# Kernel tuning notes

Measured on AMD Instinct MI355X. Metric: run time of the kernel, lower is better.

The kernel has to match this reference:

```python
import jax, jax.numpy as jnp
import numpy as np
import math

D_MODEL, D_HEAD = 1024, 64
N_HEADS = D_MODEL // D_HEAD  # 16
EPS = 1e-6

def rms_norm(x, scale, eps=EPS):
    ms = jnp.mean(x * x, axis=-1, keepdims=True)
    return x * scale * jax.lax.rsqrt(ms + eps)

def apply_rotary_emb(x, theta):
    # theta: (..., d) rotates first 2*d dims of x
    d = theta.shape[-1]
    x1, x2, x3 = x[..., :d], x[..., d:2 * d], x[..., 2 * d:]
    cos, sin = jnp.cos(theta), jnp.sin(theta)
    return jnp.concatenate([x1 * cos - x2 * sin, x2 * cos + x1 * sin, x3], axis=-1)

def make_freqs():
    d4 = D_HEAD // 4  # 16
    log_min, log_max = math.log(math.pi), math.log(10.0 * math.pi)
    f = np.exp(np.linspace(log_min, log_max, N_HEADS * d4 + 1, dtype=np.float64)[:-1])
    return jnp.asarray(f.reshape(d4, N_HEADS).T, dtype=jnp.float32)  # (n_heads, d_head//4)

def setup_inputs() -> dict:
    key = jax.random.key(0)
    ks = jax.random.split(key, 8)
    n, l = 4, 1024
    x = jax.random.normal(ks[0], (n, l, D_MODEL), jnp.float32)
    pos = jax.random.uniform(ks[1], (n, l, 2), jnp.float32)
    attn_mask = jnp.ones((1, 1, l, l), dtype=bool)
    cond = jax.random.normal(ks[2], (n, 1, D_MODEL), jnp.float32)
    norm_w = jax.random.normal(ks[3], (D_MODEL, D_MODEL), jnp.float32) * 0.02
    qkv_w = jax.random.normal(ks[4], (3 * D_MODEL, D_MODEL), jnp.float32) * (D_MODEL ** -0.5)
    qk_scale = jnp.ones((N_HEADS, 1, 1), jnp.float32)
    out_w = jax.random.normal(ks[5], (D_MODEL, D_MODEL), jnp.float32) * 0.02
    freqs = make_freqs()
    return {"x": x, "pos": pos, "attn_mask": attn_mask, "cond": cond,
            "norm_w": norm_w, "qkv_w": qkv_w, "qk_scale": qk_scale,
            "freqs": freqs, "out_w": out_w}

def reference(x, pos, attn_mask, cond, norm_w, qkv_w, qk_scale, freqs, out_w):
    n, l, d = x.shape
    # AdaRMSNorm
    h = rms_norm(x, jnp.einsum('nlc,dc->nld', cond, norm_w) + 1.0)
    # QKV projection -> (n, h, l, e)
    qkv = jnp.einsum('nld,ed->nle', h, qkv_w)
    q, k, v = jnp.split(qkv, 3, axis=-1)
    split_heads = lambda t: t.reshape(n, l, N_HEADS, D_HEAD).transpose(0, 2, 1, 3)
    q, k, v = split_heads(q), split_heads(k), split_heads(v)
    # per-head RMSNorm (scale shape (h,1,1))
    q = rms_norm(q, qk_scale)
    k = rms_norm(k, qk_scale)
    # axial RoPE: theta (n, h, l, d_head//2)
    theta = jnp.concatenate([
        pos[:, None, :, 0:1] * freqs[None, :, None, :],
        pos[:, None, :, 1:2] * freqs[None, :, None, :],
    ], axis=-1)
    q = apply_rotary_emb(q, theta)
    k = apply_rotary_emb(k, theta)
    # SDPA
    scores = jnp.einsum('nhqe,nhke->nhqk', q, k) * (D_HEAD ** -0.5)
    scores = jnp.where(attn_mask, scores, jnp.float32(-1e30))
    attn = jax.nn.softmax(scores, axis=-1)
    o = jnp.einsum('nhqk,nhke->nhqe', attn, v)
    o = o.transpose(0, 2, 1, 3).reshape(n, l, d)
    return jnp.einsum('nld,ed->nle', o, out_w)
```

## Files before the change

kernel.cpp:

```cpp
#include <hip/hip_runtime.h>

typedef short bf16x8 __attribute__((ext_vector_type(8)));
typedef float f32x4 __attribute__((ext_vector_type(4)));

__device__ __forceinline__ float bf2f(ushort u) {
  union { unsigned int i; float f; } x; x.i = ((unsigned int)u) << 16; return x.f;
}
__device__ __forceinline__ ushort f2bf(float f) {
  union { float f; unsigned int i; } x; x.f = f;
  unsigned int r = x.i + 0x7fff + ((x.i >> 16) & 1);
  return (ushort)(r >> 16);
}
__device__ __forceinline__ unsigned int cvtpk_bf16(float a, float b) {
  unsigned int r;
  asm("v_cvt_pk_bf16_f32 %0, %1, %2" : "=v"(r) : "v"(a), "v"(b));
  return r;
}

__device__ __forceinline__ f32x4 mfma16(bf16x8 a, bf16x8 b, f32x4 c) {
  return __builtin_amdgcn_mfma_f32_16x16x32_bf16(a, b, c, 0, 0, 0);
}

__device__ __forceinline__ void gload_lds16(const void* g, void* l) {
  __builtin_amdgcn_global_load_lds(
      (const __attribute__((address_space(1))) void*)g,
      (__attribute__((address_space(3))) void*)l, 16, 0, 0);
}

__global__ __launch_bounds__(256) void f2bf_vec(const float* __restrict__ in,
                                                ushort* __restrict__ out, int n4) {
  int i = blockIdx.x * 256 + threadIdx.x;
  if (i >= n4) return;
  float4 v = ((const float4*)in)[i];
  ushort4 o;
  o.x = f2bf(v.x); o.y = f2bf(v.y); o.z = f2bf(v.z); o.w = f2bf(v.w);
  ((ushort4*)out)[i] = o;
}

__global__ __launch_bounds__(256) void cond_gemv(const float* __restrict__ cond,
                                                 const float* __restrict__ nw,
                                                 float* __restrict__ sout) {
  const int w = threadIdx.x >> 6, lane = threadIdx.x & 63;
  const int idx = blockIdx.x * 4 + w;
  const int n_ = idx >> 10, d = idx & 1023;
  const float* cr = cond + n_ * 1024;
  const float* wr_ = nw + (size_t)d * 1024;
  float sum = 0.f;
#pragma unroll
  for (int c = lane; c < 1024; c += 64) sum += cr[c] * wr_[c];
#pragma unroll
  for (int off = 1; off < 64; off <<= 1) sum += __shfl_xor(sum, off);
  if (lane == 0) sout[idx] = sum + 1.0f;
}

__global__ __launch_bounds__(256) void rmsnorm_x(const float* __restrict__ x,
                                                 const float* __restrict__ s,
                                                 ushort* __restrict__ h, int L) {
  const int row = blockIdx.x;
  const int n_ = row / L;
  const int tid = threadIdx.x;
  __shared__ float red[4];
  float4 xv = ((const float4*)(x + (size_t)row * 1024))[tid];
  float ss = xv.x * xv.x + xv.y * xv.y + xv.z * xv.z + xv.w * xv.w;
#pragma unroll
  for (int off = 1; off < 64; off <<= 1) ss += __shfl_xor(ss, off);
  if ((tid & 63) == 0) red[tid >> 6] = ss;
  __syncthreads();
  float tot = red[0] + red[1] + red[2] + red[3];
  float r = rsqrtf(tot * (1.f / 1024.f) + 1e-6f);
  float4 sv = ((const float4*)(s + (size_t)n_ * 1024))[tid];
  ushort4 o;
  o.x = f2bf(xv.x * sv.x * r);
  o.y = f2bf(xv.y * sv.y * r);
  o.z = f2bf(xv.z * sv.z * r);
  o.w = f2bf(xv.w * sv.w * r);
  ((ushort4*)(h + (size_t)row * 1024))[tid] = o;
}

template <typename OT>
__global__ __launch_bounds__(256) void gemm_bt(const ushort* __restrict__ A,
                                               const ushort* __restrict__ B,
                                               OT* __restrict__ C, int M, int N,
                                               int K, int nbx) {
  __shared__ ushort As[2][128 * 32];
  __shared__ ushort Bs[2][128 * 32];
  const int tid = threadIdx.x;
  const int w = tid >> 6;
  const int lane = tid & 63;
  const int wr = w >> 1, wc = w & 1;
  const int lm = lane & 15, g = lane >> 4;
  const int qchunk = gridDim.x >> 3;
  const int swz = (blockIdx.x & 7) * qchunk + (blockIdx.x >> 3);
  const int bn = (swz % nbx) * 128;
  const int bm = (swz / nbx) * 128;
  f32x4 acc[4][4] = {};
  const int u_ = lane >> 3;
  const int pp = (lane & 7) ^ u_;
  const int srow = (u_ << 1) | (pp >> 2);
  const int scol = (pp & 3) * 8;
  const int rb = (lm >> 1) * 64 + (((((lm & 1) << 2) | g) ^ (lm >> 1)) << 3);

  auto stage = [&](int kt, int b) {
#pragma unroll
    for (int i = 0; i < 2; ++i) {
      const int c = w * 2 + i;
      gload_lds16(&A[(size_t)(bm + c * 16 + srow) * K + kt + scol],
                  &As[b][c * 512]);
      gload_lds16(&B[(size_t)(bn + c * 16 + srow) * K + kt + scol],
                  &Bs[b][c * 512]);
    }
  };

  const int NTK = K >> 5;
  stage(0, 0);
  stage(32, 1);
  for (int t = 0; t < NTK; ++t) {
    const int b = t & 1;
    if (t + 1 < NTK)
      asm volatile("s_waitcnt vmcnt(4)" ::: "memory");
    else
      asm volatile("s_waitcnt vmcnt(0)" ::: "memory");
    __builtin_amdgcn_s_barrier();
    bf16x8 af[4], bfr[4];
#pragma unroll
    for (int mi = 0; mi < 4; ++mi)
      af[mi] = *(const bf16x8*)&As[b][(wr * 4 + mi) * 512 + rb];
#pragma unroll
    for (int ni = 0; ni < 4; ++ni)
      bfr[ni] = *(const bf16x8*)&Bs[b][(wc * 4 + ni) * 512 + rb];
    asm volatile("s_waitcnt lgkmcnt(0)" ::: "memory");
    __builtin_amdgcn_sched_barrier(0);
    __builtin_amdgcn_s_barrier();
    if (t + 2 < NTK) stage((t + 2) << 5, b);
#pragma unroll
    for (int mi = 0; mi < 4; ++mi)
#pragma unroll
      for (int ni = 0; ni < 4; ++ni)
        acc[mi][ni] = mfma16(af[mi], bfr[ni], acc[mi][ni]);
  }
#pragma unroll
  for (int mi = 0; mi < 4; ++mi)
#pragma unroll
    for (int ni = 0; ni < 4; ++ni) {
      int col = bn + wc * 64 + ni * 16 + lm;
#pragma unroll
      for (int r = 0; r < 4; ++r) {
        int row = bm + wr * 64 + mi * 16 + g * 4 + r;
        float v = acc[mi][ni][r];
        if constexpr (sizeof(OT) == 2)
          C[(size_t)row * N + col] = (OT)f2bf(v);
        else
          C[(size_t)row * N + col] = (OT)v;
      }
    }
}

__global__ __launch_bounds__(256) void qkv_prep(
    const ushort* __restrict__ qkv, const float* __restrict__ pos,
    const float* __restrict__ qscale, const float* __restrict__ freqs,
    ushort* __restrict__ Qr, ushort* __restrict__ Kr, ushort* __restrict__ Vr,
    int L) {
  const int row = blockIdx.x;
  const int n_ = row / L;
  const int l = row - n_ * L;
  const int w = threadIdx.x >> 6, lane = threadIdx.x & 63;
  const float p0 = pos[row * 2 + 0], p1 = pos[row * 2 + 1];
  const int tl = lane & 31;
#pragma unroll
  for (int hi = 0; hi < 4; ++hi) {
    const int h = w * 4 + hi;
    const size_t ib = (size_t)row * 3072 + h * 64 + lane;
    float qv = bf2f(qkv[ib]);
    float kv = bf2f(qkv[ib + 1024]);
    float vv = bf2f(qkv[ib + 2048]);
    float sq = qv * qv, sk = kv * kv;
#pragma unroll
    for (int off = 1; off < 64; off <<= 1) {
      sq += __shfl_xor(sq, off);
      sk += __shfl_xor(sk, off);
    }
    const float sc = qscale[h];
    float qn = qv * sc * rsqrtf(sq * (1.f / 64.f) + 1e-6f);
    float kn = kv * sc * rsqrtf(sk * (1.f / 64.f) + 1e-6f);
    float th = ((tl < 16) ? p0 : p1) * freqs[h * 16 + (tl & 15)];
    float s_, c_;
    sincosf(th, &s_, &c_);
    float qo = __shfl_xor(qn, 32);
    float ko = __shfl_xor(kn, 32);
    float qr = (lane < 32) ? (qn * c_ - qo * s_) : (qn * c_ + qo * s_);
    float kr = (lane < 32) ? (kn * c_ - ko * s_) : (kn * c_ + ko * s_);
    const size_t ob = ((size_t)(n_ * 16 + h) * L + l) * 64 + lane;
    Qr[ob] = f2bf(qr * 0.18033688f);
    Kr[ob] = f2bf(kr);
    Vr[ob] = f2bf(vv);
  }
}

__global__ __launch_bounds__(256) void vtrans(const ushort* __restrict__ v,
                                              ushort* __restrict__ vt) {
  __shared__ ushort T[64][72];
  const int tid = threadIdx.x;
  const int nh = blockIdx.y;
  const int l0 = blockIdx.x * 64;
  const int lr = tid >> 2;
  const int d0 = (tid & 3) * 16;
  const ushort* src = v + ((size_t)nh * 1024 + l0 + lr) * 64 + d0;
  *(uint4*)&T[lr][d0] = *(const uint4*)src;
  *(uint4*)&T[lr][d0 + 8] = *(const uint4*)(src + 8);
  __syncthreads();
  const int d = tid >> 2;
  const int lc = (tid & 3) * 16;
  ushort tmp[16];
#pragma unroll
  for (int j = 0; j < 16; ++j) tmp[j] = T[lc + j][d];
  ushort* dst = vt + ((size_t)nh * 64 + d) * 1024 + l0 + lc;
  *(uint4*)dst = *(uint4*)&tmp[0];
  *(uint4*)(dst + 8) = *(uint4*)&tmp[8];
}

__global__ __launch_bounds__(256) void attn_kernel(
    const ushort* __restrict__ Q, const ushort* __restrict__ Kg,
    const ushort* __restrict__ Vtg, ushort* __restrict__ O, int L) {
  __shared__ ushort Ks[2][64 * 64];
  __shared__ ushort Vs[2][64 * 64];
  __shared__ ushort Pb[4][16 * 64];
  const int tid = threadIdx.x;
  const int w = tid >> 6, lane = tid & 63;
  const int lm = lane & 15, g = lane >> 4;
  const int swz = (blockIdx.x & 7) * 128 + (blockIdx.x >> 3);
  const int nh = swz >> 4;
  const int qt = swz & 15;
  const ushort* q = Q + (size_t)nh * L * 64;
  const ushort* k = Kg + (size_t)nh * L * 64;
  const ushort* vt = Vtg + (size_t)nh * 64 * L;
  const int qbase = qt * 64 + w * 16;
  bf16x8 qf[2];
#pragma unroll
  for (int kc = 0; kc < 2; ++kc)
    qf[kc] = *(const bf16x8*)&q[(size_t)(qbase + lm) * 64 + kc * 32 + g * 8];
  f32x4 ot[4] = {};
  f32x4 lsacc = {};
  bf16x8 ones;
#pragma unroll
  for (int i = 0; i < 8; ++i) ones[i] = (short)0x3F80;
  const int sr = lane >> 3;
  const int ss = (lane & 7) ^ sr;

  auto stage = [&](int tt, int b) {
#pragma unroll
    for (int i = 0; i < 2; ++i) {
      const int r = w * 16 + i * 8 + sr;
      gload_lds16(&k[(size_t)(tt * 64 + r) * 64 + ss * 8],
                  &Ks[b][(w * 16 + i * 8) * 64]);
    }
#pragma unroll
    for (int i = 0; i < 2; ++i) {
      const int r = w * 16 + i * 8 + sr;
      gload_lds16(&vt[(size_t)r * L + tt * 64 + ss * 8],
                  &Vs[b][(w * 16 + i * 8) * 64]);
    }
  };

  stage(0, 0);
  __syncthreads();
  const int NT = L >> 6;
  for (int t = 0; t < NT; ++t) {
    const int cur = t & 1;
    if (t + 1 < NT) stage(t + 1, cur ^ 1);
    const ushort* ksb = &Ks[cur][0];
    f32x4 st[4] = {};
    __builtin_amdgcn_s_setprio(1);
#pragma unroll
    for (int t16 = 0; t16 < 4; ++t16) {
      const int r = t16 * 16 + lm;
#pragma unroll
      for (int kc = 0; kc < 2; ++kc) {
        bf16x8 a = *(const bf16x8*)&ksb[r * 64 + (((kc * 4 + g) ^ (lm & 7)) << 3)];
        st[t16] = mfma16(a, qf[kc], st[t16]);
      }
    }
    __builtin_amdgcn_s_setprio(0);
    float e[4][4];
#pragma unroll
    for (int t16 = 0; t16 < 4; ++t16)
#pragma unroll
      for (int r = 0; r < 4; ++r)
        e[t16][r] = __builtin_amdgcn_exp2f(st[t16][r]);
    ushort* pb = &Pb[w][0];
#pragma unroll
    for (int t16 = 0; t16 < 4; ++t16) {
      unsigned int lo = cvtpk_bf16(e[t16][0], e[t16][1]);
      unsigned int hi = cvtpk_bf16(e[t16][2], e[t16][3]);
      const int slot = (t16 * 2 + (g >> 1)) ^ (lm & 7);
      *(uint2*)&pb[lm * 64 + slot * 8 + (g & 1) * 4] = make_uint2(lo, hi);
    }
    asm volatile("s_waitcnt lgkmcnt(0)" ::: "memory");
    __builtin_amdgcn_sched_barrier(0);
    bf16x8 pf[2];
#pragma unroll
    for (int c = 0; c < 2; ++c)
      pf[c] = *(const bf16x8*)&pb[lm * 64 + (((c * 4 + g) ^ (lm & 7)) << 3)];
    const ushort* vsb = &Vs[cur][0];
    __builtin_amdgcn_s_setprio(1);
#pragma unroll
    for (int db = 0; db < 4; ++db) {
      const int d = db * 16 + lm;
#pragma unroll
      for (int c = 0; c < 2; ++c) {
        bf16x8 a = *(const bf16x8*)&vsb[d * 64 + (((c * 4 + g) ^ (lm & 7)) << 3)];
        ot[db] = mfma16(a, pf[c], ot[db]);
      }
    }
#pragma unroll
    for (int c = 0; c < 2; ++c) lsacc = mfma16(ones, pf[c], lsacc);
    __builtin_amdgcn_s_setprio(0);
    __syncthreads();
  }
  const float inv = 1.f / lsacc[0];
  const int n_ = nh >> 4, h = nh & 15;
#pragma unroll
  for (int db = 0; db < 4; ++db) {
    unsigned int lo = cvtpk_bf16(ot[db][0] * inv, ot[db][1] * inv);
    unsigned int hi = cvtpk_bf16(ot[db][2] * inv, ot[db][3] * inv);
    size_t off =
        ((size_t)(n_ * L + qbase + lm) * 1024) + h * 64 + db * 16 + g * 4;
    *(uint2*)&O[off] = make_uint2(lo, hi);
  }
}

extern "C" void kernel_launch(void* const* d_in, const int* in_sizes, int n_in,
                              void* d_out, int out_size, void* d_ws,
                              size_t ws_size, hipStream_t stream) {
  const float* x = (const float*)d_in[0];
  const float* pos = (const float*)d_in[1];
  const float* cond = (const float*)d_in[3];
  const float* norm_w = (const float*)d_in[4];
  const float* qkv_w = (const float*)d_in[5];
  const float* qk_scale = (const float*)d_in[6];
  const float* freqs = (const float*)d_in[7];
  const float* out_w = (const float*)d_in[8];
  float* out = (float*)d_out;
  const int L = 1024;

  char* wsb = (char*)d_ws;
  ushort* qkvw_bf = (ushort*)(wsb);
  ushort* outw_bf = (ushort*)(wsb + 6291456);
  float* s_cond = (float*)(wsb + 8388608);
  ushort* h_buf = (ushort*)(wsb + 8404992);
  ushort* qkv_buf = (ushort*)(wsb + 16793600);
  ushort* q_r = (ushort*)(wsb + 41959424);
  ushort* k_r = (ushort*)(wsb + 50348032);
  ushort* v_r = (ushort*)(wsb + 58736640);
  ushort* o_buf = (ushort*)(wsb + 67125248);
  ushort* vt_buf = h_buf;

  hipLaunchKernelGGL(f2bf_vec, dim3(3072), dim3(256), 0, stream, qkv_w,
                     qkvw_bf, 786432);
  hipLaunchKernelGGL(f2bf_vec, dim3(1024), dim3(256), 0, stream, out_w,
                     outw_bf, 262144);
  hipLaunchKernelGGL(cond_gemv, dim3(1024), dim3(256), 0, stream, cond, norm_w,
                     s_cond);
  hipLaunchKernelGGL(rmsnorm_x, dim3(4096), dim3(256), 0, stream, x, s_cond,
                     h_buf, L);
  hipLaunchKernelGGL(gemm_bt<ushort>, dim3(768), dim3(256), 0, stream, h_buf,
                     qkvw_bf, qkv_buf, 4096, 3072, 1024, 24);
  hipLaunchKernelGGL(qkv_prep, dim3(4096), dim3(256), 0, stream, qkv_buf, pos,
                     qk_scale, freqs, q_r, k_r, v_r, L);
  hipLaunchKernelGGL(vtrans, dim3(16, 64), dim3(256), 0, stream, v_r, vt_buf);
  hipLaunchKernelGGL(attn_kernel, dim3(1024), dim3(256), 0, stream, q_r, k_r,
                     vt_buf, o_buf, L);
  hipLaunchKernelGGL(gemm_bt<float>, dim3(256), dim3(256), 0, stream, o_buf,
                     outw_bf, out, 4096, 1024, 1024, 8);
}
```

Baseline: 126.1 us.

## Process 32 query rows per wave in attention and merge weight conversions

The attention kernel now handles two 16-row query sub-tiles per wave (128 queries per block), so each K and V fragment read from LDS feeds two MFMAs and the K/V tiles are staged from global memory half as often. The grid shrinks from 1024 to 512 blocks, the block swizzle is adjusted to match, and the per-wave P buffer doubles in size. The two fp32-to-bf16 weight conversion launches are also merged into one kernel to save a launch. The cost is higher register and LDS use per block and fewer blocks, which may reduce occupancy on the 256-CU device.

```diff
diff --git a/kernel.cpp b/kernel.cpp
--- a/kernel.cpp
+++ b/kernel.cpp
@@ -27,14 +27,25 @@
       (__attribute__((address_space(3))) void*)l, 16, 0, 0);
 }
 
-__global__ __launch_bounds__(256) void f2bf_vec(const float* __restrict__ in,
-                                                ushort* __restrict__ out, int n4) {
+__global__ __launch_bounds__(256) void f2bf_vec2(const float* __restrict__ a,
+                                                 ushort* __restrict__ oa, int n4a,
+                                                 const float* __restrict__ b,
+                                                 ushort* __restrict__ ob, int n4b) {
   int i = blockIdx.x * 256 + threadIdx.x;
-  if (i >= n4) return;
-  float4 v = ((const float4*)in)[i];
+  const float* src;
+  ushort* dst;
+  int j;
+  if (i < n4a) {
+    src = a; dst = oa; j = i;
+  } else {
+    j = i - n4a;
+    if (j >= n4b) return;
+    src = b; dst = ob;
+  }
+  float4 v = ((const float4*)src)[j];
   ushort4 o;
   o.x = f2bf(v.x); o.y = f2bf(v.y); o.z = f2bf(v.z); o.w = f2bf(v.w);
-  ((ushort4*)out)[i] = o;
+  ((ushort4*)dst)[j] = o;
 }
 
 __global__ __launch_bounds__(256) void cond_gemv(const float* __restrict__ cond,
@@ -223,23 +234,26 @@
     const ushort* __restrict__ Vtg, ushort* __restrict__ O, int L) {
   __shared__ ushort Ks[2][64 * 64];
   __shared__ ushort Vs[2][64 * 64];
-  __shared__ ushort Pb[4][16 * 64];
+  __shared__ ushort Pb[4][32 * 64];
   const int tid = threadIdx.x;
   const int w = tid >> 6, lane = tid & 63;
   const int lm = lane & 15, g = lane >> 4;
-  const int swz = (blockIdx.x & 7) * 128 + (blockIdx.x >> 3);
-  const int nh = swz >> 4;
-  const int qt = swz & 15;
+  const int swz = (blockIdx.x & 7) * 64 + (blockIdx.x >> 3);
+  const int nh = swz >> 3;
+  const int qt = swz & 7;
   const ushort* q = Q + (size_t)nh * L * 64;
   const ushort* k = Kg + (size_t)nh * L * 64;
   const ushort* vt = Vtg + (size_t)nh * 64 * L;
-  const int qbase = qt * 64 + w * 16;
-  bf16x8 qf[2];
-#pragma unroll
-  for (int kc = 0; kc < 2; ++kc)
-    qf[kc] = *(const bf16x8*)&q[(size_t)(qbase + lm) * 64 + kc * 32 + g * 8];
-  f32x4 ot[4] = {};
-  f32x4 lsacc = {};
+  const int qbase = qt * 128 + w * 32;
+  bf16x8 qf[2][2];
+#pragma unroll
+  for (int qs = 0; qs < 2; ++qs)
+#pragma unroll
+    for (int kc = 0; kc < 2; ++kc)
+      qf[qs][kc] = *(const bf16x8*)&q[(size_t)(qbase + qs * 16 + lm) * 64 +
+                                      kc * 32 + g * 8];
+  f32x4 ot[2][4] = {};
+  f32x4 lsacc[2] = {};
   bf16x8 ones;
 #pragma unroll
   for (int i = 0; i < 8; ++i) ones[i] = (short)0x3F80;
@@ -268,7 +282,7 @@
     const int cur = t & 1;
     if (t + 1 < NT) stage(t + 1, cur ^ 1);
     const ushort* ksb = &Ks[cur][0];
-    f32x4 st[4] = {};
+    f32x4 st[2][4] = {};
     __builtin_amdgcn_s_setprio(1);
 #pragma unroll
     for (int t16 = 0; t16 < 4; ++t16) {
@@ -276,30 +290,39 @@
 #pragma unroll
       for (int kc = 0; kc < 2; ++kc) {
         bf16x8 a = *(const bf16x8*)&ksb[r * 64 + (((kc * 4 + g) ^ (lm & 7)) << 3)];
-        st[t16] = mfma16(a, qf[kc], st[t16]);
+        st[0][t16] = mfma16(a, qf[0][kc], st[0][t16]);
+        st[1][t16] = mfma16(a, qf[1][kc], st[1][t16]);
       }
     }
     __builtin_amdgcn_s_setprio(0);
-    float e[4][4];
-#pragma unroll
-    for (int t16 = 0; t16 < 4; ++t16)
-#pragma unroll
-      for (int r = 0; r < 4; ++r)
-        e[t16][r] = __builtin_amdgcn_exp2f(st[t16][r]);
+    float e[2][4][4];
+#pragma unroll
+    for (int qs = 0; qs < 2; ++qs)
+#pragma unroll
+      for (int t16 = 0; t16 < 4; ++t16)
+#pragma unroll
+        for (int r = 0; r < 4; ++r)
+          e[qs][t16][r] = __builtin_amdgcn_exp2f(st[qs][t16][r]);
     ushort* pb = &Pb[w][0];
 #pragma unroll
-    for (int t16 = 0; t16 < 4; ++t16) {
-      unsigned int lo = cvtpk_bf16(e[t16][0], e[t16][1]);
-      unsigned int hi = cvtpk_bf16(e[t16][2], e[t16][3]);
-      const int slot = (t16 * 2 + (g >> 1)) ^ (lm & 7);
-      *(uint2*)&pb[lm * 64 + slot * 8 + (g & 1) * 4] = make_uint2(lo, hi);
-    }
+    for (int qs = 0; qs < 2; ++qs)
+#pragma unroll
+      for (int t16 = 0; t16 < 4; ++t16) {
+        unsigned int lo = cvtpk_bf16(e[qs][t16][0], e[qs][t16][1]);
+        unsigned int hi = cvtpk_bf16(e[qs][t16][2], e[qs][t16][3]);
+        const int slot = (t16 * 2 + (g >> 1)) ^ (lm & 7);
+        *(uint2*)&pb[(qs * 16 + lm) * 64 + slot * 8 + (g & 1) * 4] =
+            make_uint2(lo, hi);
+      }
     asm volatile("s_waitcnt lgkmcnt(0)" ::: "memory");
     __builtin_amdgcn_sched_barrier(0);
-    bf16x8 pf[2];
-#pragma unroll
-    for (int c = 0; c < 2; ++c)
-      pf[c] = *(const bf16x8*)&pb[lm * 64 + (((c * 4 + g) ^ (lm & 7)) << 3)];
+    bf16x8 pf[2][2];
+#pragma unroll
+    for (int qs = 0; qs < 2; ++qs)
+#pragma unroll
+      for (int c = 0; c < 2; ++c)
+        pf[qs][c] = *(const bf16x8*)&pb[(qs * 16 + lm) * 64 +
+                                        (((c * 4 + g) ^ (lm & 7)) << 3)];
     const ushort* vsb = &Vs[cur][0];
     __builtin_amdgcn_s_setprio(1);
 #pragma unroll
@@ -308,23 +331,30 @@
 #pragma unroll
       for (int c = 0; c < 2; ++c) {
         bf16x8 a = *(const bf16x8*)&vsb[d * 64 + (((c * 4 + g) ^ (lm & 7)) << 3)];
-        ot[db] = mfma16(a, pf[c], ot[db]);
+        ot[0][db] = mfma16(a, pf[0][c], ot[0][db]);
+        ot[1][db] = mfma16(a, pf[1][c], ot[1][db]);
       }
     }
 #pragma unroll
-    for (int c = 0; c < 2; ++c) lsacc = mfma16(ones, pf[c], lsacc);
+    for (int qs = 0; qs < 2; ++qs)
+#pragma unroll
+      for (int c = 0; c < 2; ++c)
+        lsacc[qs] = mfma16(ones, pf[qs][c], lsacc[qs]);
     __builtin_amdgcn_s_setprio(0);
     __syncthreads();
   }
-  const float inv = 1.f / lsacc[0];
   const int n_ = nh >> 4, h = nh & 15;
 #pragma unroll
-  for (int db = 0; db < 4; ++db) {
-    unsigned int lo = cvtpk_bf16(ot[db][0] * inv, ot[db][1] * inv);
-    unsigned int hi = cvtpk_bf16(ot[db][2] * inv, ot[db][3] * inv);
-    size_t off =
-        ((size_t)(n_ * L + qbase + lm) * 1024) + h * 64 + db * 16 + g * 4;
-    *(uint2*)&O[off] = make_uint2(lo, hi);
+  for (int qs = 0; qs < 2; ++qs) {
+    const float inv = 1.f / lsacc[qs][0];
+#pragma unroll
+    for (int db = 0; db < 4; ++db) {
+      unsigned int lo = cvtpk_bf16(ot[qs][db][0] * inv, ot[qs][db][1] * inv);
+      unsigned int hi = cvtpk_bf16(ot[qs][db][2] * inv, ot[qs][db][3] * inv);
+      size_t off = ((size_t)(n_ * L + qbase + qs * 16 + lm) * 1024) + h * 64 +
+                   db * 16 + g * 4;
+      *(uint2*)&O[off] = make_uint2(lo, hi);
+    }
   }
 }
 
@@ -354,10 +384,8 @@
   ushort* o_buf = (ushort*)(wsb + 67125248);
   ushort* vt_buf = h_buf;
 
-  hipLaunchKernelGGL(f2bf_vec, dim3(3072), dim3(256), 0, stream, qkv_w,
-                     qkvw_bf, 786432);
-  hipLaunchKernelGGL(f2bf_vec, dim3(1024), dim3(256), 0, stream, out_w,
-                     outw_bf, 262144);
+  hipLaunchKernelGGL(f2bf_vec2, dim3(4096), dim3(256), 0, stream, qkv_w,
+                     qkvw_bf, 786432, out_w, outw_bf, 262144);
   hipLaunchKernelGGL(cond_gemv, dim3(1024), dim3(256), 0, stream, cond, norm_w,
                      s_cond);
   hipLaunchKernelGGL(rmsnorm_x, dim3(4096), dim3(256), 0, stream, x, s_cond,
@@ -367,7 +395,7 @@
   hipLaunchKernelGGL(qkv_prep, dim3(4096), dim3(256), 0, stream, qkv_buf, pos,
                      qk_scale, freqs, q_r, k_r, v_r, L);
   hipLaunchKernelGGL(vtrans, dim3(16, 64), dim3(256), 0, stream, v_r, vt_buf);
-  hipLaunchKernelGGL(attn_kernel, dim3(1024), dim3(256), 0, stream, q_r, k_r,
+  hipLaunchKernelGGL(attn_kernel, dim3(512), dim3(256), 0, stream, q_r, k_r,
                      vt_buf, o_buf, L);
   hipLaunchKernelGGL(gemm_bt<float>, dim3(256), dim3(256), 0, stream, o_buf,
                      outw_bf, out, 4096, 1024, 1024, 8);
```

Measured after the change: 120.9 us. 4.1% less time.
